# Kernel tuning notes

Hardware: AMD Instinct MI355X
Metric: run time of the kernel (lower is better)

Reference implementation:

```python
import jax, jax.numpy as jnp
import numpy as np

NT = 128
T = 262144


def setup_inputs() -> dict:
    key = jax.random.key(0)
    k1, k2, k3, k4, k5 = jax.random.split(key, 5)
    emit = jax.random.normal(k1, (T, NT), dtype=jnp.float32)
    y = jax.random.randint(k2, (T,), 0, NT, dtype=jnp.int64)
    trans = jax.random.normal(k3, (NT, NT), dtype=jnp.float32)
    strans = jax.random.normal(k4, (NT,), dtype=jnp.float32)
    etrans = jax.random.normal(k5, (NT,), dtype=jnp.float32)
    return {"emit": emit, "y": y, "trans": trans, "strans": strans, "etrans": etrans}


def _crf_nll(emit, y, trans, strans, etrans):
    Tlen = emit.shape[0]

    # forward algorithm (log partition) via scan over timesteps 1..T-1
    alpha0 = strans + emit[0]  # [nt]

    def step(alpha, e_t):
        # alpha_new[n] = logsumexp_p(alpha[p] + trans[p, n]) + emit_t[n]
        alpha_new = jax.nn.logsumexp(alpha[:, None] + trans, axis=0) + e_t
        return alpha_new, None

    alpha, _ = jax.lax.scan(step, alpha0, emit[1:])
    logZ = jax.nn.logsumexp(alpha + etrans)

    # gold score (faithful to original: emissions indexed by the *previous* tag)
    prev = y[:-1]
    nxt = y[1:]
    score = strans[y[0]]
    score = score + jnp.sum(trans[prev, nxt] + emit[jnp.arange(Tlen - 1), prev])
    score = score + etrans[y[-1]] + emit[-1, y[-1]]

    return logZ - score


def reference(emit, y, trans, strans, etrans):
    return _crf_nll(emit, y, trans, strans, etrans)
```

## Files before the change

### kernel.cpp

```cpp
#include <hip/hip_runtime.h>

typedef _Float16 f16x4 __attribute__((ext_vector_type(4)));
typedef float    f32x4 __attribute__((ext_vector_type(4)));

#define T_LEN   262144
#define NTAG    128
#define LCH     16
#define BURN    16
#define NSTEP   (LCH + BURN)
#define NCHUNK  (T_LEN / LCH)
#define NWAVE   (NCHUNK / 16)
#define NSCOREB 256
#define NFWDB   (NWAVE / 4)
#define NBLK    (NSCOREB + NFWDB)

__global__ __launch_bounds__(256, 2) void crf_all(
    const float* __restrict__ emit, const int* __restrict__ y,
    const float* __restrict__ trans, const float* __restrict__ strans,
    const float* __restrict__ etrans, double* __restrict__ ws,
    float* __restrict__ out)
{
  if (blockIdx.x < NSCOREB) {
    __shared__ float sred[4];
    int idx0 = blockIdx.x * 256 + threadIdx.x;
    float v = 0.f;
    for (int t = idx0; t < T_LEN - 1; t += NSCOREB * 256) {
      int yt = y[t], yn = y[t + 1];
      v += trans[yt * NTAG + yn] + emit[(size_t)t * NTAG + yt];
    }
    if (idx0 == 0) {
      int yl = y[T_LEN - 1];
      v += strans[y[0]] + etrans[yl] + emit[(size_t)(T_LEN - 1) * NTAG + yl];
    }
#pragma unroll
    for (int off = 1; off < 64; off <<= 1) v += __shfl_xor(v, off, 64);
    if ((threadIdx.x & 63) == 0) sred[threadIdx.x >> 6] = v;
    __syncthreads();
    if (threadIdx.x == 0)
      atomicAdd(&ws[1], (double)(sred[0] + sred[1] + sred[2] + sred[3]));
  } else {
    const int w   = threadIdx.x >> 6;
    const int l   = threadIdx.x & 63;
    const int col = l & 15;
    const int grp = l >> 4;
    const int gw  = (blockIdx.x - NSCOREB) * 4 + w;
    const int gc  = gw * 16 + col;

    f16x4 a[8][8];
#pragma unroll
    for (int rt = 0; rt < 8; ++rt) {
      const int outtag = 16 * rt + col;
#pragma unroll
      for (int kt = 0; kt < 8; ++kt) {
        f16x4 t4;
#pragma unroll
        for (int j = 0; j < 4; ++j)
          t4[j] = (_Float16)__expf(trans[(16 * kt + 4 * grp + j) * NTAG + outtag]);
        a[rt][kt] = t4;
      }
    }

    f16x4 b[8];
    float acc = 0.f;
    if (gc == 0) {
      float al[8][4];
      float vm = -1e30f;
#pragma unroll
      for (int kt = 0; kt < 8; ++kt)
#pragma unroll
        for (int r = 0; r < 4; ++r) {
          int tag = 16 * kt + 4 * grp + r;
          al[kt][r] = strans[tag] + emit[tag];
          vm = fmaxf(vm, al[kt][r]);
        }
      vm = fmaxf(vm, __shfl_xor(vm, 16, 64));
      vm = fmaxf(vm, __shfl_xor(vm, 32, 64));
      acc = vm;
#pragma unroll
      for (int kt = 0; kt < 8; ++kt) {
        f16x4 nb;
#pragma unroll
        for (int r = 0; r < 4; ++r) nb[r] = (_Float16)__expf(al[kt][r] - vm);
        b[kt] = nb;
      }
    } else {
#pragma unroll
      for (int kt = 0; kt < 8; ++kt) {
        f16x4 nb;
#pragma unroll
        for (int r = 0; r < 4; ++r) nb[r] = (_Float16)1.0f;
        b[kt] = nb;
      }
    }

    const int row0 = (gc == 0) ? 1 : (gc * LCH - BURN);
    const float* ebase = emit + (size_t)row0 * NTAG + 4 * grp;
    float4 pf[8];
#pragma unroll
    for (int rt = 0; rt < 8; ++rt) pf[rt] = *(const float4*)(ebase + 16 * rt);
    ebase += NTAG;

#pragma unroll 1
    for (int s = 0; s < NSTEP; ++s) {
      f32x4 c[8];
#pragma unroll
      for (int rt = 0; rt < 8; ++rt) c[rt] = (f32x4){0.f, 0.f, 0.f, 0.f};
#pragma unroll
      for (int kt = 0; kt < 8; ++kt)
#pragma unroll
        for (int rt = 0; rt < 8; ++rt)
          c[rt] = __builtin_amdgcn_mfma_f32_16x16x16f16(a[rt][kt], b[kt], c[rt], 0, 0, 0);

      float e[8][4];
#pragma unroll
      for (int rt = 0; rt < 8; ++rt) {
        e[rt][0] = __expf(pf[rt].x);
        e[rt][1] = __expf(pf[rt].y);
        e[rt][2] = __expf(pf[rt].z);
        e[rt][3] = __expf(pf[rt].w);
      }
      if (s < NSTEP - 1) {
#pragma unroll
        for (int rt = 0; rt < 8; ++rt) pf[rt] = *(const float4*)(ebase + 16 * rt);
        ebase += NTAG;
      }

      float u[8][4];
      float vm = -1e30f;
#pragma unroll
      for (int rt = 0; rt < 8; ++rt)
#pragma unroll
        for (int r = 0; r < 4; ++r) {
          u[rt][r] = c[rt][r] * e[rt][r];
          vm = fmaxf(vm, u[rt][r]);
        }
      vm = fmaxf(vm, __shfl_xor(vm, 16, 64));
      vm = fmaxf(vm, __shfl_xor(vm, 32, 64));
      const float lm   = __logf(vm);
      const bool  on   = (gc == 0) ? (s <= LCH - 2) : (s >= BURN);
      if (on) acc += lm;
      const float rinv = __frcp_rn(vm);
#pragma unroll
      for (int kt = 0; kt < 8; ++kt) {
        f16x4 nb;
#pragma unroll
        for (int r = 0; r < 4; ++r) nb[r] = (_Float16)(u[kt][r] * rinv);
        b[kt] = nb;
      }

      if (s == NSTEP - 1 && gc == NCHUNK - 1) {
        float lv = 0.f;
#pragma unroll
        for (int rt = 0; rt < 8; ++rt)
#pragma unroll
          for (int r = 0; r < 4; ++r)
            lv += (u[rt][r] * rinv) * __expf(etrans[16 * rt + 4 * grp + r]);
        lv += __shfl_xor(lv, 16, 64);
        lv += __shfl_xor(lv, 32, 64);
        if (grp == 0) atomicAdd(&ws[2], (double)lv);
      }
    }

    float av = (grp == 0) ? acc : 0.f;
#pragma unroll
    for (int off = 1; off < 64; off <<= 1) av += __shfl_xor(av, off, 64);
    if (l == 0) atomicAdd(&ws[0], (double)av);
  }

  __syncthreads();
  if (threadIdx.x == 0) {
    __threadfence();
    unsigned t = atomicAdd((unsigned*)&ws[3], 1u);
    if (t == NBLK - 1) {
      double d0 = atomicAdd(&ws[0], 0.0);
      double d1 = atomicAdd(&ws[1], 0.0);
      double d2 = atomicAdd(&ws[2], 0.0);
      out[0] = (float)(d0 + log(d2) - d1);
    }
  }
}

extern "C" void kernel_launch(void* const* d_in, const int* in_sizes, int n_in,
                              void* d_out, int out_size, void* d_ws, size_t ws_size,
                              hipStream_t stream)
{
  const float* emit   = (const float*)d_in[0];
  const int*   y      = (const int*)d_in[1];
  const float* trans  = (const float*)d_in[2];
  const float* strans = (const float*)d_in[3];
  const float* etrans = (const float*)d_in[4];
  float*  out = (float*)d_out;
  double* ws  = (double*)d_ws;

  hipMemsetAsync(ws, 0, 4 * sizeof(double), stream);
  crf_all<<<dim3(NBLK), dim3(256), 0, stream>>>(
      emit, y, trans, strans, etrans, ws, out);
}
```

Measured before the change: 95.96 us.

## Use FP8 MFMA for chunked forward recursion with shorter chunks and burn-in

Switches the forward-algorithm matrix products from f16 16x16x16 MFMA to fp8 16x16x32 MFMA, packing exp(trans) and the normalized alpha vector into fp8, which halves the MFMA count per step. It also shortens chunks from 16 to 8 steps and burn-in from 16 to 12, doubling the number of chunks and waves while cutting sequential steps per wave. The fp8 precision and shorter burn-in risk accuracy of the log-partition. Forward blocks are also moved ahead of the score blocks in the grid.

```diff
diff --git a/kernel.cpp b/kernel.cpp
--- a/kernel.cpp
+++ b/kernel.cpp
@@ -1,18 +1,17 @@
 #include <hip/hip_runtime.h>
 
-typedef _Float16 f16x4 __attribute__((ext_vector_type(4)));
-typedef float    f32x4 __attribute__((ext_vector_type(4)));
+typedef float f32x4 __attribute__((ext_vector_type(4)));
 
 #define T_LEN   262144
 #define NTAG    128
-#define LCH     16
-#define BURN    16
+#define LCH     8
+#define BURN    12
 #define NSTEP   (LCH + BURN)
 #define NCHUNK  (T_LEN / LCH)
 #define NWAVE   (NCHUNK / 16)
+#define NFWDB   (NWAVE / 4)
 #define NSCOREB 256
-#define NFWDB   (NWAVE / 4)
-#define NBLK    (NSCOREB + NFWDB)
+#define NBLK    (NFWDB + NSCOREB)
 
 __global__ __launch_bounds__(256, 2) void crf_all(
     const float* __restrict__ emit, const int* __restrict__ y,
@@ -20,85 +19,76 @@
     const float* __restrict__ etrans, double* __restrict__ ws,
     float* __restrict__ out)
 {
-  if (blockIdx.x < NSCOREB) {
-    __shared__ float sred[4];
-    int idx0 = blockIdx.x * 256 + threadIdx.x;
-    float v = 0.f;
-    for (int t = idx0; t < T_LEN - 1; t += NSCOREB * 256) {
-      int yt = y[t], yn = y[t + 1];
-      v += trans[yt * NTAG + yn] + emit[(size_t)t * NTAG + yt];
-    }
-    if (idx0 == 0) {
-      int yl = y[T_LEN - 1];
-      v += strans[y[0]] + etrans[yl] + emit[(size_t)(T_LEN - 1) * NTAG + yl];
-    }
-#pragma unroll
-    for (int off = 1; off < 64; off <<= 1) v += __shfl_xor(v, off, 64);
-    if ((threadIdx.x & 63) == 0) sred[threadIdx.x >> 6] = v;
-    __syncthreads();
-    if (threadIdx.x == 0)
-      atomicAdd(&ws[1], (double)(sred[0] + sred[1] + sred[2] + sred[3]));
-  } else {
+  if (blockIdx.x < NFWDB) {
     const int w   = threadIdx.x >> 6;
     const int l   = threadIdx.x & 63;
     const int col = l & 15;
     const int grp = l >> 4;
-    const int gw  = (blockIdx.x - NSCOREB) * 4 + w;
+    const int gw  = blockIdx.x * 4 + w;
     const int gc  = gw * 16 + col;
 
-    f16x4 a[8][8];
+    long a[8][4];
 #pragma unroll
     for (int rt = 0; rt < 8; ++rt) {
       const int outtag = 16 * rt + col;
 #pragma unroll
-      for (int kt = 0; kt < 8; ++kt) {
-        f16x4 t4;
-#pragma unroll
-        for (int j = 0; j < 4; ++j)
-          t4[j] = (_Float16)__expf(trans[(16 * kt + 4 * grp + j) * NTAG + outtag]);
-        a[rt][kt] = t4;
-      }
-    }
-
-    f16x4 b[8];
+      for (int kt = 0; kt < 4; ++kt) {
+        float q[8];
+#pragma unroll
+        for (int j = 0; j < 8; ++j) {
+          const int k = 32 * kt + 4 * grp + (j & 3) + 16 * (j >> 2);
+          q[j] = __expf(trans[k * NTAG + outtag]);
+        }
+        unsigned lo = (unsigned)__builtin_amdgcn_cvt_pk_fp8_f32(q[0], q[1], 0, false);
+        lo = (unsigned)__builtin_amdgcn_cvt_pk_fp8_f32(q[2], q[3], (int)lo, true);
+        unsigned hi = (unsigned)__builtin_amdgcn_cvt_pk_fp8_f32(q[4], q[5], 0, false);
+        hi = (unsigned)__builtin_amdgcn_cvt_pk_fp8_f32(q[6], q[7], (int)hi, true);
+        a[rt][kt] = (long)(((unsigned long long)hi << 32) | lo);
+      }
+    }
+
+    float u[8][4];
     float acc = 0.f;
     if (gc == 0) {
-      float al[8][4];
       float vm = -1e30f;
 #pragma unroll
-      for (int kt = 0; kt < 8; ++kt)
+      for (int rt = 0; rt < 8; ++rt)
 #pragma unroll
         for (int r = 0; r < 4; ++r) {
-          int tag = 16 * kt + 4 * grp + r;
-          al[kt][r] = strans[tag] + emit[tag];
-          vm = fmaxf(vm, al[kt][r]);
+          const int tag = 16 * rt + 4 * grp + r;
+          u[rt][r] = strans[tag] + emit[tag];
+          vm = fmaxf(vm, u[rt][r]);
         }
       vm = fmaxf(vm, __shfl_xor(vm, 16, 64));
       vm = fmaxf(vm, __shfl_xor(vm, 32, 64));
       acc = vm;
 #pragma unroll
-      for (int kt = 0; kt < 8; ++kt) {
-        f16x4 nb;
-#pragma unroll
-        for (int r = 0; r < 4; ++r) nb[r] = (_Float16)__expf(al[kt][r] - vm);
-        b[kt] = nb;
-      }
+      for (int rt = 0; rt < 8; ++rt)
+#pragma unroll
+        for (int r = 0; r < 4; ++r) u[rt][r] = __expf(u[rt][r] - vm);
     } else {
 #pragma unroll
-      for (int kt = 0; kt < 8; ++kt) {
-        f16x4 nb;
-#pragma unroll
-        for (int r = 0; r < 4; ++r) nb[r] = (_Float16)1.0f;
-        b[kt] = nb;
-      }
-    }
-
-    const int row0 = (gc == 0) ? 1 : (gc * LCH - BURN);
-    const float* ebase = emit + (size_t)row0 * NTAG + 4 * grp;
+      for (int rt = 0; rt < 8; ++rt)
+#pragma unroll
+        for (int r = 0; r < 4; ++r) u[rt][r] = 1.0f;
+    }
+    long b[4];
+#pragma unroll
+    for (int kt = 0; kt < 4; ++kt) {
+      unsigned lo = (unsigned)__builtin_amdgcn_cvt_pk_fp8_f32(u[2*kt][0], u[2*kt][1], 0, false);
+      lo = (unsigned)__builtin_amdgcn_cvt_pk_fp8_f32(u[2*kt][2], u[2*kt][3], (int)lo, true);
+      unsigned hi = (unsigned)__builtin_amdgcn_cvt_pk_fp8_f32(u[2*kt+1][0], u[2*kt+1][1], 0, false);
+      hi = (unsigned)__builtin_amdgcn_cvt_pk_fp8_f32(u[2*kt+1][2], u[2*kt+1][3], (int)hi, true);
+      b[kt] = (long)(((unsigned long long)hi << 32) | lo);
+    }
+
+    const int t0 = (gc == 0) ? 1 : (gc * LCH - BURN);
     float4 pf[8];
-#pragma unroll
-    for (int rt = 0; rt < 8; ++rt) pf[rt] = *(const float4*)(ebase + 16 * rt);
-    ebase += NTAG;
+    {
+      const float* ep = emit + ((size_t)max(t0, 0) << 7) + 4 * grp;
+#pragma unroll
+      for (int rt = 0; rt < 8; ++rt) pf[rt] = *(const float4*)(ep + 16 * rt);
+    }
 
 #pragma unroll 1
     for (int s = 0; s < NSTEP; ++s) {
@@ -106,10 +96,10 @@
 #pragma unroll
       for (int rt = 0; rt < 8; ++rt) c[rt] = (f32x4){0.f, 0.f, 0.f, 0.f};
 #pragma unroll
-      for (int kt = 0; kt < 8; ++kt)
+      for (int kt = 0; kt < 4; ++kt)
 #pragma unroll
         for (int rt = 0; rt < 8; ++rt)
-          c[rt] = __builtin_amdgcn_mfma_f32_16x16x16f16(a[rt][kt], b[kt], c[rt], 0, 0, 0);
+          c[rt] = __builtin_amdgcn_mfma_f32_16x16x32_fp8_fp8(a[rt][kt], b[kt], c[rt], 0, 0, 0);
 
       float e[8][4];
 #pragma unroll
@@ -120,12 +110,12 @@
         e[rt][3] = __expf(pf[rt].w);
       }
       if (s < NSTEP - 1) {
-#pragma unroll
-        for (int rt = 0; rt < 8; ++rt) pf[rt] = *(const float4*)(ebase + 16 * rt);
-        ebase += NTAG;
-      }
-
-      float u[8][4];
+        const int tn = t0 + s + 1;
+        const float* ep = emit + ((size_t)max(tn, 0) << 7) + 4 * grp;
+#pragma unroll
+        for (int rt = 0; rt < 8; ++rt) pf[rt] = *(const float4*)(ep + 16 * rt);
+      }
+
       float vm = -1e30f;
 #pragma unroll
       for (int rt = 0; rt < 8; ++rt)
@@ -136,16 +126,20 @@
         }
       vm = fmaxf(vm, __shfl_xor(vm, 16, 64));
       vm = fmaxf(vm, __shfl_xor(vm, 32, 64));
-      const float lm   = __logf(vm);
-      const bool  on   = (gc == 0) ? (s <= LCH - 2) : (s >= BURN);
-      if (on) acc += lm;
+      const bool on = (gc == 0) ? (s <= LCH - 2) : (s >= BURN);
+      if (on) acc += __logf(vm);
       const float rinv = __frcp_rn(vm);
 #pragma unroll
-      for (int kt = 0; kt < 8; ++kt) {
-        f16x4 nb;
-#pragma unroll
-        for (int r = 0; r < 4; ++r) nb[r] = (_Float16)(u[kt][r] * rinv);
-        b[kt] = nb;
+      for (int kt = 0; kt < 4; ++kt) {
+        float s0 = u[2*kt][0] * rinv,   s1 = u[2*kt][1] * rinv;
+        float s2 = u[2*kt][2] * rinv,   s3 = u[2*kt][3] * rinv;
+        float s4 = u[2*kt+1][0] * rinv, s5 = u[2*kt+1][1] * rinv;
+        float s6 = u[2*kt+1][2] * rinv, s7 = u[2*kt+1][3] * rinv;
+        unsigned lo = (unsigned)__builtin_amdgcn_cvt_pk_fp8_f32(s0, s1, 0, false);
+        lo = (unsigned)__builtin_amdgcn_cvt_pk_fp8_f32(s2, s3, (int)lo, true);
+        unsigned hi = (unsigned)__builtin_amdgcn_cvt_pk_fp8_f32(s4, s5, 0, false);
+        hi = (unsigned)__builtin_amdgcn_cvt_pk_fp8_f32(s6, s7, (int)hi, true);
+        b[kt] = (long)(((unsigned long long)hi << 32) | lo);
       }
 
       if (s == NSTEP - 1 && gc == NCHUNK - 1) {
@@ -157,7 +151,7 @@
             lv += (u[rt][r] * rinv) * __expf(etrans[16 * rt + 4 * grp + r]);
         lv += __shfl_xor(lv, 16, 64);
         lv += __shfl_xor(lv, 32, 64);
-        if (grp == 0) atomicAdd(&ws[2], (double)lv);
+        if (l == 15) atomicAdd(&ws[2], (double)lv);
       }
     }
 
@@ -165,6 +159,24 @@
 #pragma unroll
     for (int off = 1; off < 64; off <<= 1) av += __shfl_xor(av, off, 64);
     if (l == 0) atomicAdd(&ws[0], (double)av);
+  } else {
+    __shared__ float sred[4];
+    int idx0 = (blockIdx.x - NFWDB) * 256 + threadIdx.x;
+    float v = 0.f;
+    for (int t = idx0; t < T_LEN - 1; t += NSCOREB * 256) {
+      int yt = y[t], yn = y[t + 1];
+      v += trans[yt * NTAG + yn] + emit[(size_t)t * NTAG + yt];
+    }
+    if (idx0 == 0) {
+      int yl = y[T_LEN - 1];
+      v += strans[y[0]] + etrans[yl] + emit[(size_t)(T_LEN - 1) * NTAG + yl];
+    }
+#pragma unroll
+    for (int off = 1; off < 64; off <<= 1) v += __shfl_xor(v, off, 64);
+    if ((threadIdx.x & 63) == 0) sred[threadIdx.x >> 6] = v;
+    __syncthreads();
+    if (threadIdx.x == 0)
+      atomicAdd(&ws[1], (double)(sred[0] + sred[1] + sred[2] + sred[3]));
   }
 
   __syncthreads();
```

After: 105.9 us. 1.1x slower.
